# Performance work log

Hardware: AMD Instinct MI355X
Metric: run time of the kernel (lower is better)

The kernel has to match this reference:

```python
import jax, jax.numpy as jnp
import numpy as np

N_SPANS = 4096
EMB_DIM = 384
HEADS = 4
DECAY_LAMBDA = 5.0
THRESHOLD = 0.1
NEG_SLOPE = 0.2  # PyG GATConv default leaky_relu slope


def setup_inputs() -> dict:
    key = jax.random.key(0)
    k1, k2, k3, k4, k5, k6 = jax.random.split(key, 6)
    embeddings = jax.random.normal(k1, (N_SPANS, EMB_DIM), dtype=jnp.float32)
    span_positions = jnp.sort(
        jax.random.randint(k2, (N_SPANS, 2), 0, 100000), axis=1
    ).astype(jnp.int64)
    # GATConv params: lin (no bias), per-head attention vectors, output bias
    glorot = 1.0 / np.sqrt(EMB_DIM)
    W = jax.random.normal(k3, (EMB_DIM, HEADS, EMB_DIM), dtype=jnp.float32) * glorot
    att_src = jax.random.normal(k4, (HEADS, EMB_DIM), dtype=jnp.float32) * glorot
    att_dst = jax.random.normal(k5, (HEADS, EMB_DIM), dtype=jnp.float32) * glorot
    bias = jnp.zeros((EMB_DIM,), dtype=jnp.float32)
    return {
        "embeddings": embeddings,
        "span_positions": span_positions,
        "W": W,
        "att_src": att_src,
        "att_dst": att_dst,
        "bias": bias,
    }


def _adjacency_mask(embeddings):
    # A_ij = cos_sim(e_i, e_j) * exp(-|i - j| / lambda); edges where A > 0.1
    n = embeddings.shape[0]
    en = embeddings / jnp.linalg.norm(embeddings, axis=1, keepdims=True)
    cos_sim = en @ en.T  # [N, N]
    idx = jnp.arange(n, dtype=embeddings.dtype)
    decay = jnp.exp(-jnp.abs(idx[None, :] - idx[:, None]) / DECAY_LAMBDA)
    adj = cos_sim * decay
    # diagonal is 1.0 > threshold, so self-loops (required by GATConv) are present
    return adj > THRESHOLD  # symmetric mask: mask[i, j] == edge j -> i


def reference(embeddings, span_positions, W, att_src, att_dst, bias):
    mask = _adjacency_mask(embeddings)  # [N_dst, N_src]
    # GATConv(heads=4, concat=False): project, per-head additive attention
    x = jnp.einsum("nd,dhe->nhe", embeddings, W)  # [N, H, E]
    a_src = jnp.einsum("nhe,he->nh", x, att_src)  # [N, H]
    a_dst = jnp.einsum("nhe,he->nh", x, att_dst)  # [N, H]
    # logits[i, j, h] for edge j -> i
    logits = jax.nn.leaky_relu(a_dst[:, None, :] + a_src[None, :, :], NEG_SLOPE)
    logits = jnp.where(mask[:, :, None], logits, jnp.float32(-jnp.inf))
    alpha = jax.nn.softmax(logits, axis=1)  # softmax over incoming sources j
    out = jnp.einsum("ijh,jhe->ihe", alpha, x)  # [N, H, E]
    out = out.mean(axis=1) + bias  # concat=False -> mean over heads, then bias
    return out
```

## Files before the change

### kernel.cpp

```cpp
#include <hip/hip_runtime.h>
#include <hip/hip_bf16.h>
#include <math.h>

#define N_SPANS 4096
#define EMB 384
#define HEADS 4
#define HE (HEADS * EMB)
#define BAND 11
#define BW (2 * BAND + 1)

typedef short bf16x8 __attribute__((ext_vector_type(8)));
typedef short bf16x4 __attribute__((ext_vector_type(4)));
typedef float f32x4 __attribute__((ext_vector_type(4)));

__device__ __forceinline__ unsigned short f2bf(float f) {
    union { float f; unsigned u; } x; x.f = f;
    unsigned r = x.u + 0x7fffu + ((x.u >> 16) & 1u);
    return (unsigned short)(r >> 16);
}
__device__ __forceinline__ float bf2f(unsigned short u) {
    union { unsigned u; float f; } x; x.u = ((unsigned)u) << 16; return x.f;
}

__device__ __forceinline__ float wave_sum(float v) {
    #pragma unroll
    for (int off = 32; off; off >>= 1) v += __shfl_xor(v, off, 64);
    return v;
}
__device__ __forceinline__ float wave_max(float v) {
    #pragma unroll
    for (int off = 32; off; off >>= 1) v = fmaxf(v, __shfl_xor(v, off, 64));
    return v;
}

__device__ __forceinline__ bf16x4 pack4(float a, float b, float c, float d) {
    bf16x4 r;
    r[0] = (short)f2bf(a); r[1] = (short)f2bf(b);
    r[2] = (short)f2bf(c); r[3] = (short)f2bf(d);
    return r;
}

__global__ __launch_bounds__(256) void mega(const float* __restrict__ E,
                                            const float* __restrict__ W,
                                            const float* __restrict__ attS,
                                            const float* __restrict__ attD,
                                            unsigned short* __restrict__ Xb,
                                            float* __restrict__ invn,
                                            float* __restrict__ Dots,
                                            float* __restrict__ asrcP,
                                            float* __restrict__ adstP) {
    __shared__ unsigned short As[128 * 32];
    __shared__ unsigned short Bs[128 * 32];
    __shared__ float sAS[128], sAD[128];
    const int b = blockIdx.x;
    const int tid = threadIdx.x;
    const int lane = tid & 63, w = tid >> 6;

    if (b < 384) {
        const int nt = b % 12;
        const int m0 = (b / 12) * 128;
        const int n0 = nt * 128;
        const int wave = w;
        const int quad = lane >> 4;
        const int l16 = lane & 15;
        const int wr = (wave >> 1) * 64;
        const int wc = (wave & 1) * 64;

        if (tid < 128) { sAS[tid] = 0.f; sAD[tid] = 0.f; }

        const int kAe = (tid & 7) * 4;
        const int rA = tid >> 3;
        const int sA = (rA >> 1) & 3;
        const int cA = kAe >> 3;
        const unsigned aByte = rA * 64 + ((cA ^ sA) * 16) + (tid & 1) * 8;
        const float* Ag = E + (size_t)(m0 + rA) * EMB + kAe;

        const int gB = tid & 31, kgB = tid >> 5;
        const float* Bg = W + (size_t)(kgB * 4) * HE + n0 + gB * 4;

        const int rchunk = (quad ^ ((l16 >> 1) & 3)) * 16;

        f32x4 acc[4][4];
        #pragma unroll
        for (int i = 0; i < 4; ++i)
            #pragma unroll
            for (int j = 0; j < 4; ++j) acc[i][j] = 0.f;

        float4 fa[4], fb[4];
        #pragma unroll
        for (int q = 0; q < 4; ++q)
            fa[q] = *(const float4*)(Ag + (size_t)q * 32 * EMB);
        #pragma unroll
        for (int i = 0; i < 4; ++i)
            fb[i] = *(const float4*)(Bg + (size_t)i * HE);

        for (int kt = 0; kt < 12; ++kt) {
            #pragma unroll
            for (int q = 0; q < 4; ++q)
                *(bf16x4*)((char*)As + q * 2048 + aByte) =
                    pack4(fa[q].x, fa[q].y, fa[q].z, fa[q].w);
            #pragma unroll
            for (int j = 0; j < 4; ++j) {
                const int c = gB * 4 + j;
                const int sB = (c >> 1) & 3;
                *(bf16x4*)((char*)Bs + c * 64 + (((kgB >> 1) ^ sB) * 16) + (kgB & 1) * 8) =
                    pack4((&fb[0].x)[j], (&fb[1].x)[j], (&fb[2].x)[j], (&fb[3].x)[j]);
            }
            __syncthreads();

            if (kt < 11) {
                const int ko = (kt + 1) * 32;
                #pragma unroll
                for (int q = 0; q < 4; ++q)
                    fa[q] = *(const float4*)(Ag + (size_t)q * 32 * EMB + ko);
                #pragma unroll
                for (int i = 0; i < 4; ++i)
                    fb[i] = *(const float4*)(Bg + (size_t)(ko + i) * HE);
            }

            bf16x8 af[4], bfr[4];
            #pragma unroll
            for (int t = 0; t < 4; ++t) {
                af[t]  = *(const bf16x8*)((const char*)As + (wr + t * 16 + l16) * 64 + rchunk);
                bfr[t] = *(const bf16x8*)((const char*)Bs + (wc + t * 16 + l16) * 64 + rchunk);
            }
            #pragma unroll
            for (int ti = 0; ti < 4; ++ti)
                #pragma unroll
                for (int tj = 0; tj < 4; ++tj)
                    acc[ti][tj] = __builtin_amdgcn_mfma_f32_16x16x32_bf16(
                        af[ti], bfr[tj], acc[ti][tj], 0, 0, 0);

            __syncthreads();
        }

        float aS[4], aD[4];
        #pragma unroll
        for (int tj = 0; tj < 4; ++tj) {
            int col = n0 + wc + tj * 16 + l16;
            aS[tj] = attS[col];
            aD[tj] = attD[col];
        }
        #pragma unroll
        for (int ti = 0; ti < 4; ++ti)
            #pragma unroll
            for (int r = 0; r < 4; ++r) {
                float ps = 0.f, pd = 0.f;
                #pragma unroll
                for (int tj = 0; tj < 4; ++tj) {
                    float v = acc[ti][tj][r];
                    ps += v * aS[tj];
                    pd += v * aD[tj];
                }
                #pragma unroll
                for (int off = 1; off < 16; off <<= 1) {
                    ps += __shfl_xor(ps, off, 64);
                    pd += __shfl_xor(pd, off, 64);
                }
                if (l16 == 0) {
                    int lrow = wr + ti * 16 + quad * 4 + r;
                    atomicAdd(&sAS[lrow], ps);
                    atomicAdd(&sAD[lrow], pd);
                }
            }
        __syncthreads();
        {
            const int p = nt % 3, h = nt / 3;
            if (tid < 128)
                asrcP[((size_t)p * N_SPANS + m0 + tid) * HEADS + h] = sAS[tid];
            else
                adstP[((size_t)p * N_SPANS + m0 + tid - 128) * HEADS + h] = sAD[tid - 128];
        }

        #pragma unroll
        for (int ti = 0; ti < 4; ++ti)
            #pragma unroll
            for (int tj = 0; tj < 4; ++tj) {
                int col = n0 + wc + tj * 16 + l16;
                #pragma unroll
                for (int r = 0; r < 4; ++r) {
                    int row = m0 + wr + ti * 16 + quad * 4 + r;
                    Xb[row * HE + col] = f2bf(acc[ti][tj][r]);
                }
            }
    } else {
        const int n = (b - 384) * 4 + w;
        const float4* er4 = (const float4*)(E + (size_t)n * EMB);
        const int dmax = (n >= N_SPANS - BAND) ? (N_SPANS - 1 - n) : BAND;
        const float4* nb4[BAND];
        #pragma unroll
        for (int d = 1; d <= BAND; ++d) {
            int j = n + d; if (j > N_SPANS - 1) j = N_SPANS - 1;
            nb4[d - 1] = (const float4*)(E + (size_t)j * EMB);
        }
        float acc[12];
        #pragma unroll
        for (int d = 0; d < 12; ++d) acc[d] = 0.f;
        #pragma unroll
        for (int mq = 0; mq < 2; ++mq) {
            const int idx = mq * 64 + lane;
            if (idx < 96) {
                float4 v = er4[idx];
                acc[0] += v.x * v.x + v.y * v.y + v.z * v.z + v.w * v.w;
                #pragma unroll
                for (int d = 1; d <= BAND; ++d) {
                    float4 u = nb4[d - 1][idx];
                    float dd = v.x * u.x + v.y * u.y + v.z * u.z + v.w * u.w;
                    acc[d] += (d <= dmax) ? dd : 0.f;
                }
            }
        }
        #pragma unroll
        for (int d = 0; d < 12; ++d) acc[d] = wave_sum(acc[d]);
        float dval = 0.f;
        #pragma unroll
        for (int d = 1; d <= BAND; ++d) if (lane == d) dval = acc[d];
        if (lane >= 1 && lane <= BAND) Dots[(size_t)n * 12 + lane] = dval;
        if (lane == 0) invn[n] = 1.0f / sqrtf(acc[0]);
    }
}

__global__ __launch_bounds__(256) void band_attn(const float* __restrict__ invn,
                                                 const float* __restrict__ Dots,
                                                 const float* __restrict__ asrcP,
                                                 const float* __restrict__ adstP,
                                                 const unsigned short* __restrict__ Xb,
                                                 const float* __restrict__ bias,
                                                 float* __restrict__ out) {
    __shared__ float sAl[4][BW][4];
    __shared__ int sList[4][24];
    const int tid = threadIdx.x, lane = tid & 63, w = tid >> 6;
    const int i = blockIdx.x * 4 + w;
    const int jo = lane;
    const int j = i - BAND + jo;
    const bool inb = (jo < BW) && (j >= 0) && (j < N_SPANS);
    const int jc = inb ? j : i;

    float dotv = 0.f;
    if (inb) {
        if (jo < BAND)      dotv = Dots[(size_t)j * 12 + (BAND - jo)];
        else if (jo > BAND) dotv = Dots[(size_t)i * 12 + (jo - BAND)];
    }
    bool flag;
    if (jo == BAND) {
        flag = true;
    } else {
        int dd = jo < BAND ? BAND - jo : jo - BAND;
        float a = ((dotv * invn[i]) * invn[jc]) * expf(-(float)dd * 0.2f);
        flag = inb && (a > 0.1f);
    }

    unsigned long long mbits = __ballot(flag);
    const int cnt = __popcll(mbits);
    const int rank = __popcll(mbits & ((1ull << jo) - 1ull));
    if (flag) sList[w][rank] = jo;

    const float4* S4 = (const float4*)asrcP;
    const float4* D4 = (const float4*)adstP;
    float4 ad, as;
    {
        float4 a0 = D4[i], a1 = D4[N_SPANS + i], a2 = D4[2 * N_SPANS + i];
        ad = make_float4(a0.x + a1.x + a2.x, a0.y + a1.y + a2.y,
                         a0.z + a1.z + a2.z, a0.w + a1.w + a2.w);
        if (inb) {
            float4 s0 = S4[jc], s1 = S4[N_SPANS + jc], s2 = S4[2 * N_SPANS + jc];
            as = make_float4(s0.x + s1.x + s2.x, s0.y + s1.y + s2.y,
                             s0.z + s1.z + s2.z, s0.w + s1.w + s2.w);
        } else {
            as = make_float4(0.f, 0.f, 0.f, 0.f);
        }
    }
    float al[4];
    #pragma unroll
    for (int h = 0; h < 4; ++h) {
        float z = (&ad.x)[h] + (&as.x)[h];
        z = (z >= 0.f) ? z : 0.2f * z;
        float lg = flag ? z : -INFINITY;
        float mx = wave_max(lg);
        float ex = flag ? expf(lg - mx) : 0.f;
        float sm = wave_sum(ex);
        al[h] = ex / sm;
    }
    if (flag) *(float4*)&sAl[w][jo][0] = make_float4(al[0], al[1], al[2], al[3]);

    #pragma unroll
    for (int mq = 0; mq < 2; ++mq) {
        const int e4 = mq * 64 + lane;
        if (e4 < 96) {
            float4 a = make_float4(0.f, 0.f, 0.f, 0.f);
            for (int ii = 0; ii < cnt; ++ii) {
                const int joL = sList[w][ii];
                const int jj = i - BAND + joL;
                const float4 a4 = *(const float4*)&sAl[w][joL][0];
                const ushort4* xr = (const ushort4*)(Xb + (size_t)jj * HE);
                ushort4 h0 = xr[e4], h1 = xr[e4 + 96], h2 = xr[e4 + 192], h3 = xr[e4 + 288];
                a.x += a4.x * bf2f(h0.x) + a4.y * bf2f(h1.x) + a4.z * bf2f(h2.x) + a4.w * bf2f(h3.x);
                a.y += a4.x * bf2f(h0.y) + a4.y * bf2f(h1.y) + a4.z * bf2f(h2.y) + a4.w * bf2f(h3.y);
                a.z += a4.x * bf2f(h0.z) + a4.y * bf2f(h1.z) + a4.z * bf2f(h2.z) + a4.w * bf2f(h3.z);
                a.w += a4.x * bf2f(h0.w) + a4.y * bf2f(h1.w) + a4.z * bf2f(h2.w) + a4.w * bf2f(h3.w);
            }
            const float4 bv = ((const float4*)bias)[e4];
            float4 o;
            o.x = 0.25f * a.x + bv.x;
            o.y = 0.25f * a.y + bv.y;
            o.z = 0.25f * a.z + bv.z;
            o.w = 0.25f * a.w + bv.w;
            ((float4*)(out + (size_t)i * EMB))[e4] = o;
        }
    }
}

extern "C" void kernel_launch(void* const* d_in, const int* in_sizes, int n_in,
                              void* d_out, int out_size, void* d_ws, size_t ws_size,
                              hipStream_t stream) {
    const float* E       = (const float*)d_in[0];
    const float* W       = (const float*)d_in[2];
    const float* att_src = (const float*)d_in[3];
    const float* att_dst = (const float*)d_in[4];
    const float* bias    = (const float*)d_in[5];
    float* out = (float*)d_out;

    char* ws = (char*)d_ws;
    unsigned short* Xb = (unsigned short*)ws;
    float* invn        = (float*)(ws + 12582912);
    float* Dots        = (float*)(ws + 12599296);
    float* asrcP       = (float*)(ws + 12795904);
    float* adstP       = (float*)(ws + 12992512);

    mega<<<1408, 256, 0, stream>>>(E, W, att_src, att_dst, Xb, invn, Dots, asrcP, adstP);
    band_attn<<<1024, 256, 0, stream>>>(invn, Dots, asrcP, adstP, Xb, bias, out);
}
```

Before: 99.55 us.

## Double-buffer GEMM LDS tiles and remap block indices for XCD locality

Result: slower. 103.1 us (+3.6%).

```diff
diff --git a/kernel.cpp b/kernel.cpp
--- a/kernel.cpp
+++ b/kernel.cpp
@@ -49,16 +49,17 @@
                                             float* __restrict__ Dots,
                                             float* __restrict__ asrcP,
                                             float* __restrict__ adstP) {
-    __shared__ unsigned short As[128 * 32];
-    __shared__ unsigned short Bs[128 * 32];
+    __shared__ unsigned short As[2][128 * 32];
+    __shared__ unsigned short Bs[2][128 * 32];
     __shared__ float sAS[128], sAD[128];
     const int b = blockIdx.x;
     const int tid = threadIdx.x;
     const int lane = tid & 63, w = tid >> 6;
 
     if (b < 384) {
-        const int nt = b % 12;
-        const int m0 = (b / 12) * 128;
+        const int mt = b % 32;
+        const int nt = b / 32;
+        const int m0 = mt * 128;
         const int n0 = nt * 128;
         const int wave = w;
         const int quad = lane >> 4;
@@ -87,29 +88,56 @@
             for (int j = 0; j < 4; ++j) acc[i][j] = 0.f;
 
         float4 fa[4], fb[4];
-        #pragma unroll
-        for (int q = 0; q < 4; ++q)
-            fa[q] = *(const float4*)(Ag + (size_t)q * 32 * EMB);
-        #pragma unroll
-        for (int i = 0; i < 4; ++i)
-            fb[i] = *(const float4*)(Bg + (size_t)i * HE);
-
-        for (int kt = 0; kt < 12; ++kt) {
+
+        #pragma unroll
+        for (int q = 0; q < 4; ++q) fa[q] = *(const float4*)(Ag + (size_t)q * 32 * EMB);
+        #pragma unroll
+        for (int i = 0; i < 4; ++i) fb[i] = *(const float4*)(Bg + (size_t)i * HE);
+        {
             #pragma unroll
             for (int q = 0; q < 4; ++q)
-                *(bf16x4*)((char*)As + q * 2048 + aByte) =
+                *(bf16x4*)((char*)As[0] + q * 2048 + aByte) =
                     pack4(fa[q].x, fa[q].y, fa[q].z, fa[q].w);
             #pragma unroll
             for (int j = 0; j < 4; ++j) {
                 const int c = gB * 4 + j;
                 const int sB = (c >> 1) & 3;
-                *(bf16x4*)((char*)Bs + c * 64 + (((kgB >> 1) ^ sB) * 16) + (kgB & 1) * 8) =
+                *(bf16x4*)((char*)Bs[0] + c * 64 + (((kgB >> 1) ^ sB) * 16) + (kgB & 1) * 8) =
                     pack4((&fb[0].x)[j], (&fb[1].x)[j], (&fb[2].x)[j], (&fb[3].x)[j]);
             }
-            __syncthreads();
+        }
+        #pragma unroll
+        for (int q = 0; q < 4; ++q) fa[q] = *(const float4*)(Ag + (size_t)q * 32 * EMB + 32);
+        #pragma unroll
+        for (int i = 0; i < 4; ++i) fb[i] = *(const float4*)(Bg + (size_t)(32 + i) * HE);
+        __syncthreads();
+
+        for (int kt = 0; kt < 12; ++kt) {
+            const char* aBase = (const char*)As[kt & 1];
+            const char* bBase = (const char*)Bs[kt & 1];
+            bf16x8 af[4], bfr[4];
+            #pragma unroll
+            for (int t = 0; t < 4; ++t) {
+                af[t]  = *(const bf16x8*)(aBase + (wr + t * 16 + l16) * 64 + rchunk);
+                bfr[t] = *(const bf16x8*)(bBase + (wc + t * 16 + l16) * 64 + rchunk);
+            }
 
             if (kt < 11) {
-                const int ko = (kt + 1) * 32;
+                const int nbuf = (kt + 1) & 1;
+                #pragma unroll
+                for (int q = 0; q < 4; ++q)
+                    *(bf16x4*)((char*)As[nbuf] + q * 2048 + aByte) =
+                        pack4(fa[q].x, fa[q].y, fa[q].z, fa[q].w);
+                #pragma unroll
+                for (int j = 0; j < 4; ++j) {
+                    const int c = gB * 4 + j;
+                    const int sB = (c >> 1) & 3;
+                    *(bf16x4*)((char*)Bs[nbuf] + c * 64 + (((kgB >> 1) ^ sB) * 16) + (kgB & 1) * 8) =
+                        pack4((&fb[0].x)[j], (&fb[1].x)[j], (&fb[2].x)[j], (&fb[3].x)[j]);
+                }
+            }
+            if (kt < 10) {
+                const int ko = (kt + 2) * 32;
                 #pragma unroll
                 for (int q = 0; q < 4; ++q)
                     fa[q] = *(const float4*)(Ag + (size_t)q * 32 * EMB + ko);
@@ -118,12 +146,6 @@
                     fb[i] = *(const float4*)(Bg + (size_t)(ko + i) * HE);
             }
 
-            bf16x8 af[4], bfr[4];
-            #pragma unroll
-            for (int t = 0; t < 4; ++t) {
-                af[t]  = *(const bf16x8*)((const char*)As + (wr + t * 16 + l16) * 64 + rchunk);
-                bfr[t] = *(const bf16x8*)((const char*)Bs + (wc + t * 16 + l16) * 64 + rchunk);
-            }
             #pragma unroll
             for (int ti = 0; ti < 4; ++ti)
                 #pragma unroll
@@ -184,7 +206,9 @@
                 }
             }
     } else {
-        const int n = (b - 384) * 4 + w;
+        const int db = b - 384;
+        const int nb = (db & 7) * 128 + (db >> 3);
+        const int n = nb * 4 + w;
         const float4* er4 = (const float4*)(E + (size_t)n * EMB);
         const int dmax = (n >= N_SPANS - BAND) ? (N_SPANS - 1 - n) : BAND;
         const float4* nb4[BAND];
@@ -230,7 +254,9 @@
     __shared__ float sAl[4][BW][4];
     __shared__ int sList[4][24];
     const int tid = threadIdx.x, lane = tid & 63, w = tid >> 6;
-    const int i = blockIdx.x * 4 + w;
+    const int bb = blockIdx.x;
+    const int ib = (bb & 7) * 128 + (bb >> 3);
+    const int i = ib * 4 + w;
     const int jo = lane;
     const int j = i - BAND + jo;
     const bool inb = (jo < BW) && (j >= 0) && (j < N_SPANS);
```
